# Performance work log

Measured on AMD Instinct MI355X. Metric: run time of the kernel, lower is better.

Reference implementation:

```python
import jax, jax.numpy as jnp
import numpy as np
import math

N_SCALES = 8
WAVELET_LEN = 64
MIN_SCALE, MAX_SCALE = 1.0, 64.0
BATCH, SEQ, FEAT = 16, 4096, 64


def _morlet_init():
    # Faithful to _initialize_mother_wavelets
    t = np.linspace(-4.0, 4.0, WAVELET_LEN, dtype=np.float32)
    w = np.zeros((N_SCALES, WAVELET_LEN), dtype=np.float32)
    for i in range(N_SCALES):
        omega = 2.0 + i * 0.5
        sigma = 1.0 + i * 0.1
        wav = np.exp(-t ** 2 / (2 * sigma ** 2)) * np.cos(omega * t)
        w[i] = wav / np.linalg.norm(wav)
    return jnp.asarray(w)


def setup_inputs() -> dict:
    key = jax.random.key(0)
    k1, _ = jax.random.split(key)
    signal = jax.random.normal(k1, (BATCH, SEQ, FEAT), dtype=jnp.float32)
    mother_wavelets = _morlet_init()
    scale_weights = jnp.ones((N_SCALES,), dtype=jnp.float32)
    return {"signal": signal, "mother_wavelets": mother_wavelets, "scale_weights": scale_weights}


def _scales():
    return np.logspace(math.log10(MIN_SCALE), math.log10(MAX_SCALE), N_SCALES)


def _dilate(wavelet, scale):
    # F.interpolate(mode='linear', align_corners=True) to length int(WAVELET_LEN*scale)
    L_out = int(WAVELET_LEN * scale)
    if L_out > 1:
        pos = jnp.arange(L_out, dtype=jnp.float32) * ((WAVELET_LEN - 1) / (L_out - 1))
    else:
        pos = jnp.zeros((1,), dtype=jnp.float32)
    grid = jnp.arange(WAVELET_LEN, dtype=jnp.float32)
    return jnp.interp(pos, grid, wavelet) / math.sqrt(scale)


def reference(signal, mother_wavelets, scale_weights):
    # signal: (B, S, F) -> coefficients: (B, n_scales, S, F)
    B, S, F = signal.shape
    sig = jnp.swapaxes(signal, 1, 2)  # (B, F, S): batch all FFTs over b,f per scale
    scales = _scales()
    coeffs = []
    for i in range(N_SCALES):
        s = float(scales[i])
        w = _dilate(mother_wavelets[i], s)  # (L_dil,)
        n = S + w.shape[0] - 1
        n_fft = 2 ** int(math.ceil(math.log2(n)))
        Sf = jnp.fft.rfft(sig, n=n_fft, axis=-1)
        Wf = jnp.fft.rfft(w, n=n_fft)
        conv = jnp.fft.irfft(Sf * Wf, n=n_fft, axis=-1)[..., :S]  # (B, F, S)
        coeffs.append(conv)
    C = jnp.stack(coeffs, axis=1)            # (B, n_scales, F, S)
    C = jnp.swapaxes(C, 2, 3)                # (B, n_scales, S, F)
    return C * scale_weights[None, :, None, None]
```

## Files before the change

kernel.cpp:

```cpp
#include <hip/hip_runtime.h>
#include <hip/hip_bf16.h>
#include <math.h>

typedef __attribute__((ext_vector_type(8))) short bf16x8;
typedef __attribute__((ext_vector_type(4))) float f32x4;

#define NSC    8
#define SLEN   4096
#define FEAT   64
#define CHUNK_B 8192
#define NQ     258
#define ATAB_B (NQ * 8 * 1024)

constexpr int L_[NSC]    = {64, 115, 210, 380, 689, 1248, 2261, 4096};
constexpr int CACT_[NSC] = {3, 5, 8, 13, 23, 40, 72, 129};

struct WavP { float step[NSC]; float isq[NSC]; };

__global__ void k_build_atab(const float* __restrict__ mw, const float* __restrict__ sw,
                             __hip_bfloat16* __restrict__ at, WavP wp)
{
  int e = blockIdx.x * 256 + threadIdx.x;
  int j = e & 7, l = (e >> 3) & 63, s = (e >> 9) & 7, q = e >> 12;
  int k = 16 * q - 32 + (l & 15) - 8 * (l >> 4) - j;
  float val = 0.f;
  if (k >= 0 && k < L_[s]) {
    float pos = (float)k * wp.step[s];
    int ii = (int)pos;
    float r;
    if (ii >= 63) r = mw[s * 64 + 63];
    else {
      float a = mw[s * 64 + ii];
      r = fmaf(pos - (float)ii, mw[s * 64 + ii + 1] - a, a);
    }
    val = r * wp.isq[s] * sw[s];
  }
  at[e] = __float2bfloat16(val);
}

__global__ __launch_bounds__(256) void k_transpose(const float* __restrict__ sig,
                                                   __hip_bfloat16* __restrict__ sigT2)
{
  __shared__ float t[4096];
  const int tid = threadIdx.x;
  const float* sp = sig + (size_t)blockIdx.x * 4096;
  for (int idx = tid; idx < 4096; idx += 256) {
    int r = idx >> 6, f = idx & 63;
    t[(r << 6) + (f ^ ((r & 7) << 3))] = sp[idx];
  }
  __syncthreads();
  __hip_bfloat16* op = sigT2 + (size_t)blockIdx.x * 4096;
  for (int e = tid; e < 4096; e += 256) {
    int h = e >> 11, n = (e >> 9) & 3, l = (e >> 3) & 63, i = e & 7;
    int f = n * 16 + (l & 15);
    int r = h * 32 + (l >> 4) * 8 + i;
    op[e] = __float2bfloat16(t[(r << 6) + (f ^ ((r & 7) << 3))]);
  }
}

__global__ __launch_bounds__(256, 2) void k_wavelet_mfma(
    const __hip_bfloat16* __restrict__ sigT2,
    const __hip_bfloat16* __restrict__ atab,
    float* __restrict__ out)
{
  const int tid = threadIdx.x;
  const int bid = blockIdx.x;
  const int tt  = 63 - (bid >> 4);
  const int b   = bid & 15;
  const int t0  = tt * 64;
  const int tw  = tid >> 6;
  const int l   = tid & 63;
  const int fl  = tid & 15;
  const int g   = (tid >> 4) & 3;

  const int C = tt + 1;
  const char* cb = (const char*)sigT2 + ((size_t)(b * 64 + tt)) * CHUNK_B
                   + (size_t)l * 16;
  const char* aw = (const char*)atab + tw * 8192 + (size_t)l * 16;

  f32x4 acc[NSC][4];
  const f32x4 z = {0.f, 0.f, 0.f, 0.f};
  #pragma unroll
  for (int s = 0; s < NSC; ++s)
    #pragma unroll
    for (int n = 0; n < 4; ++n) acc[s][n] = z;

  auto loadB = [&](int c, int h, bf16x8* B) {
    const char* p = cb - (size_t)c * CHUNK_B + h * 4096;
    #pragma unroll
    for (int n = 0; n < 4; ++n)
      B[n] = *(const bf16x8*)(p + n * 1024);
  };

  auto compute = [&](int c_old, const bf16x8* Bf) {
    const char* pa = aw + (size_t)c_old * 16384;
    bf16x8 Af[NSC];
    #pragma unroll
    for (int s = 0; s < NSC; ++s)
      if (c_old <= CACT_[s])
        Af[s] = *(const bf16x8*)(pa + s * 1024);
    __builtin_amdgcn_s_setprio(1);
    #pragma unroll
    for (int s = NSC - 1; s >= 0; --s) {
      if (c_old <= CACT_[s]) {
        acc[s][0] = __builtin_amdgcn_mfma_f32_16x16x32_bf16(Af[s], Bf[0], acc[s][0], 0, 0, 0);
        acc[s][1] = __builtin_amdgcn_mfma_f32_16x16x32_bf16(Af[s], Bf[1], acc[s][1], 0, 0, 0);
        acc[s][2] = __builtin_amdgcn_mfma_f32_16x16x32_bf16(Af[s], Bf[2], acc[s][2], 0, 0, 0);
        acc[s][3] = __builtin_amdgcn_mfma_f32_16x16x32_bf16(Af[s], Bf[3], acc[s][3], 0, 0, 0);
      }
    }
    __builtin_amdgcn_s_setprio(0);
  };

  bf16x8 B0[4], B1[4];
  loadB(0, 1, B0);

  for (int c = 0; c < C; ++c) {
    loadB(c, 0, B1);
    compute(2 * c, B0);
    loadB(c + 1, 1, B0);
    compute(2 * c + 1, B1);
  }

  const int trow = t0 + tw * 16 + g * 4;
  float* ob = out + (size_t)b * NSC * SLEN * FEAT;
  #pragma unroll
  for (int s = 0; s < NSC; ++s) {
    float* os = ob + (size_t)s * SLEN * FEAT;
    #pragma unroll
    for (int n = 0; n < 4; ++n)
      #pragma unroll
      for (int r = 0; r < 4; ++r)
        os[(size_t)(trow + r) * FEAT + n * 16 + fl] = acc[s][n][r];
  }
}

extern "C" void kernel_launch(void* const* d_in, const int* in_sizes, int n_in,
                              void* d_out, int out_size, void* d_ws, size_t ws_size,
                              hipStream_t stream) {
  const float* sig = (const float*)d_in[0];
  const float* mw  = (const float*)d_in[1];
  const float* sw  = (const float*)d_in[2];
  float*       out = (float*)d_out;

  __hip_bfloat16* atab  = (__hip_bfloat16*)d_ws;
  __hip_bfloat16* sigT2 = (__hip_bfloat16*)((char*)d_ws + 0x220000);

  WavP wp;
  const double lg = log10(64.0), st = lg / 7.0;
  for (int i = 0; i < NSC; ++i) {
    double y = (i == 7) ? lg : (double)i * st;
    double s = pow(10.0, y);
    wp.step[i] = (float)(63.0 / (double)(L_[i] - 1));
    wp.isq[i]  = (float)(1.0 / sqrt(s));
  }

  k_build_atab<<<NQ * 8 * 512 / 256, 256, 0, stream>>>(mw, sw, atab, wp);
  k_transpose<<<1024, 256, 0, stream>>>(sig, sigT2);
  k_wavelet_mfma<<<1024, 256, 0, stream>>>(sigT2, atab, out);
}
```

Before: 98.80 us.

## Split scale accumulation into two passes to cut registers and raise occupancy

The main MFMA kernel now accumulates the eight scales in two passes of four (long scales first, then the short scales over a limited number of steps), which halves the live accumulator registers and allows launch bounds of three blocks per SM instead of two. The A-table loads are now double-buffered alongside the B loads in a unified step loop. The A table is enlarged slightly so prefetches past the end stay in bounds. In exchange the signal chunks are read from memory twice for the first few steps, and there is extra loop overhead.

```diff
diff --git a/kernel.cpp b/kernel.cpp
--- a/kernel.cpp
+++ b/kernel.cpp
@@ -8,8 +8,7 @@
 #define NSC    8
 #define SLEN   4096
 #define FEAT   64
-#define CHUNK_B 8192
-#define NQ     258
+#define NQ     264
 #define ATAB_B (NQ * 8 * 1024)
 
 constexpr int L_[NSC]    = {64, 115, 210, 380, 689, 1248, 2261, 4096};
@@ -58,7 +57,72 @@
   }
 }
 
-__global__ __launch_bounds__(256, 2) void k_wavelet_mfma(
+template<int SB>
+__device__ __forceinline__ void loadA4(const char* aw, int c_old, bf16x8* A) {
+  #pragma unroll
+  for (int i = 0; i < 4; ++i)
+    if (c_old <= CACT_[SB + i])
+      A[i] = *(const bf16x8*)(aw + (size_t)c_old * 16384 + (SB + i) * 1024);
+}
+
+__device__ __forceinline__ void loadB4(const char* cb2, int c_old, bf16x8* B) {
+  const char* p = cb2 - (size_t)c_old * 4096;
+  #pragma unroll
+  for (int n = 0; n < 4; ++n)
+    B[n] = *(const bf16x8*)(p + n * 1024);
+}
+
+template<int SB>
+__device__ __forceinline__ void stepMFMA(int c_old, const bf16x8* A, const bf16x8* B,
+                                         f32x4 (*acc)[4]) {
+  __builtin_amdgcn_s_setprio(1);
+  #pragma unroll
+  for (int i = 3; i >= 0; --i) {
+    if (c_old <= CACT_[SB + i]) {
+      acc[i][0] = __builtin_amdgcn_mfma_f32_16x16x32_bf16(A[i], B[0], acc[i][0], 0, 0, 0);
+      acc[i][1] = __builtin_amdgcn_mfma_f32_16x16x32_bf16(A[i], B[1], acc[i][1], 0, 0, 0);
+      acc[i][2] = __builtin_amdgcn_mfma_f32_16x16x32_bf16(A[i], B[2], acc[i][2], 0, 0, 0);
+      acc[i][3] = __builtin_amdgcn_mfma_f32_16x16x32_bf16(A[i], B[3], acc[i][3], 0, 0, 0);
+    }
+  }
+  __builtin_amdgcn_s_setprio(0);
+}
+
+template<int SB>
+__device__ __forceinline__ void run_pass(const char* aw, const char* cb2, int nsteps,
+                                         float* ob, int trow, int fl) {
+  f32x4 acc[4][4];
+  const f32x4 z = {0.f, 0.f, 0.f, 0.f};
+  #pragma unroll
+  for (int i = 0; i < 4; ++i)
+    #pragma unroll
+    for (int n = 0; n < 4; ++n) acc[i][n] = z;
+
+  bf16x8 A0[4], A1[4], B0[4], B1[4];
+  loadA4<SB>(aw, 0, A0);
+  loadB4(cb2, 0, B0);
+
+  for (int st = 0; st < nsteps; st += 2) {
+    loadA4<SB>(aw, st + 1, A1);
+    loadB4(cb2, st + 1, B1);
+    stepMFMA<SB>(st, A0, B0, acc);
+    loadA4<SB>(aw, st + 2, A0);
+    loadB4(cb2, st + 2, B0);
+    stepMFMA<SB>(st + 1, A1, B1, acc);
+  }
+
+  #pragma unroll
+  for (int i = 0; i < 4; ++i) {
+    float* os = ob + (size_t)(SB + i) * SLEN * FEAT;
+    #pragma unroll
+    for (int n = 0; n < 4; ++n)
+      #pragma unroll
+      for (int r = 0; r < 4; ++r)
+        os[(size_t)(trow + r) * FEAT + n * 16 + fl] = acc[i][n][r];
+  }
+}
+
+__global__ __launch_bounds__(256, 3) void k_wavelet_mfma(
     const __hip_bfloat16* __restrict__ sigT2,
     const __hip_bfloat16* __restrict__ atab,
     float* __restrict__ out)
@@ -74,65 +138,15 @@
   const int g   = (tid >> 4) & 3;
 
   const int C = tt + 1;
-  const char* cb = (const char*)sigT2 + ((size_t)(b * 64 + tt)) * CHUNK_B
-                   + (size_t)l * 16;
-  const char* aw = (const char*)atab + tw * 8192 + (size_t)l * 16;
+  const char* aw  = (const char*)atab + tw * 8192 + (size_t)l * 16;
+  const char* cb2 = (const char*)sigT2 + ((size_t)((b * 64 + tt) * 2 + 1)) * 4096
+                    + (size_t)l * 16;
 
-  f32x4 acc[NSC][4];
-  const f32x4 z = {0.f, 0.f, 0.f, 0.f};
-  #pragma unroll
-  for (int s = 0; s < NSC; ++s)
-    #pragma unroll
-    for (int n = 0; n < 4; ++n) acc[s][n] = z;
+  float* ob = out + (size_t)b * NSC * SLEN * FEAT;
+  const int trow = t0 + tw * 16 + g * 4;
 
-  auto loadB = [&](int c, int h, bf16x8* B) {
-    const char* p = cb - (size_t)c * CHUNK_B + h * 4096;
-    #pragma unroll
-    for (int n = 0; n < 4; ++n)
-      B[n] = *(const bf16x8*)(p + n * 1024);
-  };
-
-  auto compute = [&](int c_old, const bf16x8* Bf) {
-    const char* pa = aw + (size_t)c_old * 16384;
-    bf16x8 Af[NSC];
-    #pragma unroll
-    for (int s = 0; s < NSC; ++s)
-      if (c_old <= CACT_[s])
-        Af[s] = *(const bf16x8*)(pa + s * 1024);
-    __builtin_amdgcn_s_setprio(1);
-    #pragma unroll
-    for (int s = NSC - 1; s >= 0; --s) {
-      if (c_old <= CACT_[s]) {
-        acc[s][0] = __builtin_amdgcn_mfma_f32_16x16x32_bf16(Af[s], Bf[0], acc[s][0], 0, 0, 0);
-        acc[s][1] = __builtin_amdgcn_mfma_f32_16x16x32_bf16(Af[s], Bf[1], acc[s][1], 0, 0, 0);
-        acc[s][2] = __builtin_amdgcn_mfma_f32_16x16x32_bf16(Af[s], Bf[2], acc[s][2], 0, 0, 0);
-        acc[s][3] = __builtin_amdgcn_mfma_f32_16x16x32_bf16(Af[s], Bf[3], acc[s][3], 0, 0, 0);
-      }
-    }
-    __builtin_amdgcn_s_setprio(0);
-  };
-
-  bf16x8 B0[4], B1[4];
-  loadB(0, 1, B0);
-
-  for (int c = 0; c < C; ++c) {
-    loadB(c, 0, B1);
-    compute(2 * c, B0);
-    loadB(c + 1, 1, B0);
-    compute(2 * c + 1, B1);
-  }
-
-  const int trow = t0 + tw * 16 + g * 4;
-  float* ob = out + (size_t)b * NSC * SLEN * FEAT;
-  #pragma unroll
-  for (int s = 0; s < NSC; ++s) {
-    float* os = ob + (size_t)s * SLEN * FEAT;
-    #pragma unroll
-    for (int n = 0; n < 4; ++n)
-      #pragma unroll
-      for (int r = 0; r < 4; ++r)
-        os[(size_t)(trow + r) * FEAT + n * 16 + fl] = acc[s][n][r];
-  }
+  run_pass<4>(aw, cb2, 2 * C, ob, trow, fl);
+  run_pass<0>(aw, cb2, min(2 * C, 14), ob, trow, fl);
 }
 
 extern "C" void kernel_launch(void* const* d_in, const int* in_sizes, int n_in,
@@ -144,7 +158,7 @@
   float*       out = (float*)d_out;
 
   __hip_bfloat16* atab  = (__hip_bfloat16*)d_ws;
-  __hip_bfloat16* sigT2 = (__hip_bfloat16*)((char*)d_ws + 0x220000);
+  __hip_bfloat16* sigT2 = (__hip_bfloat16*)((char*)d_ws + 0x240000);
 
   WavP wp;
   const double lg = log10(64.0), st = lg / 7.0;
@@ -155,7 +169,7 @@
     wp.isq[i]  = (float)(1.0 / sqrt(s));
   }
 
-  k_build_atab<<<NQ * 8 * 512 / 256, 256, 0, stream>>>(mw, sw, atab, wp);
+  k_build_atab<<<NQ * 16, 256, 0, stream>>>(mw, sw, atab, wp);
   k_transpose<<<1024, 256, 0, stream>>>(sig, sigT2);
   k_wavelet_mfma<<<1024, 256, 0, stream>>>(sigT2, atab, out);
 }
```

After: 90.07 us. -8.8%, faster.
